# Kernel tuning notes

Hardware: AMD Instinct MI355X
Metric: run time of the kernel (lower is better)

The kernel has to match this reference:

```python
import jax, jax.numpy as jnp
import numpy as np

B, S, HID = 2, 2048, 1024
H, HKV, D = 16, 8, 128
G = H // HKV
EPS = 1e-6
ROPE_BASE = 1e6


def _rms_norm(x, w):
    # per-last-dim RMSNorm in fp32, matching QwenRMSNorm
    x32 = x.astype(jnp.float32)
    var = jnp.mean(x32 * x32, axis=-1, keepdims=True)
    return w * (x32 * jax.lax.rsqrt(var + EPS)).astype(x.dtype)


def _rotate_half(x):
    half = x.shape[-1] // 2
    return jnp.concatenate([-x[..., half:], x[..., :half]], axis=-1)


def setup_inputs() -> dict:
    key = jax.random.key(0)
    ks = jax.random.split(key, 6)
    return {
        "hidden_states": jax.random.normal(ks[0], (B, S, HID), dtype=jnp.float32),
        "position_ids": jnp.arange(S, dtype=jnp.int32),
        "Wq": jax.random.normal(ks[1], (HID, H * D), dtype=jnp.float32) * 0.02,
        "Wk": jax.random.normal(ks[2], (HID, HKV * D), dtype=jnp.float32) * 0.02,
        "Wv": jax.random.normal(ks[3], (HID, HKV * D), dtype=jnp.float32) * 0.02,
        "Wo": jax.random.normal(ks[4], (H * D, HID), dtype=jnp.float32) * 0.02,
        "q_norm_w": jnp.ones((D,), dtype=jnp.float32),
        "k_norm_w": jnp.ones((D,), dtype=jnp.float32),
    }


def reference(hidden_states, position_ids, Wq, Wk, Wv, Wo, q_norm_w, k_norm_w):
    b, s, _ = hidden_states.shape
    # projections
    q = (hidden_states @ Wq).reshape(b, s, H, D)
    k = (hidden_states @ Wk).reshape(b, s, HKV, D)
    v = (hidden_states @ Wv).reshape(b, s, HKV, D)
    # QK RMSNorm (per head_dim), then [B, heads, S, D]
    q = _rms_norm(q, q_norm_w).transpose(0, 2, 1, 3)
    k = _rms_norm(k, k_norm_w).transpose(0, 2, 1, 3)
    v = v.transpose(0, 2, 1, 3)
    # RoPE
    inv_freq = 1.0 / (ROPE_BASE ** (jnp.arange(0, D, 2, dtype=jnp.float32) / D))
    freqs = position_ids.astype(jnp.float32)[:, None] * inv_freq[None, :]  # [S, D/2]
    emb = jnp.concatenate([freqs, freqs], axis=-1)  # [S, D]
    cos = jnp.cos(emb)[None, None, :, :].astype(q.dtype)
    sin = jnp.sin(emb)[None, None, :, :].astype(q.dtype)
    q = q * cos + _rotate_half(q) * sin
    k = k * cos + _rotate_half(k) * sin
    # GQA attention without materializing repeated K/V:
    # q heads h = kh*G + g  <->  repeat_interleave(G, dim=1) of kv heads
    qg = q.reshape(b, HKV, G, s, D)
    scale = 1.0 / jnp.sqrt(jnp.asarray(D, dtype=q.dtype))
    scores = jnp.einsum('bhgqd,bhkd->bhgqk', qg, k) * scale  # [B,HKV,G,S,S]
    causal = jnp.tril(jnp.ones((s, s), dtype=bool))
    scores = jnp.where(causal[None, None, None, :, :], scores, jnp.finfo(scores.dtype).min)
    probs = jax.nn.softmax(scores, axis=-1)
    attn = jnp.einsum('bhgqk,bhkd->bhgqd', probs, v)  # [B,HKV,G,S,D]
    attn = attn.reshape(b, H, s, D).transpose(0, 2, 1, 3).reshape(b, s, H * D)
    out = attn @ Wo
    return out, k, v
```

## Files before the change

### kernel.cpp

```cpp
#include <hip/hip_runtime.h>

#define B_ 2
#define S_ 2048
#define HID_ 1024
#define H_ 16
#define HKV_ 8
#define D_ 128

typedef unsigned short u16;
typedef __attribute__((ext_vector_type(8))) short short8;
typedef __attribute__((ext_vector_type(4))) float f32x4;
typedef __attribute__((ext_vector_type(16))) float f32x16;
typedef __attribute__((ext_vector_type(2))) unsigned short u16x2;
typedef __attribute__((ext_vector_type(4))) unsigned short u16x4;
typedef const __attribute__((address_space(1))) void gvoid;
typedef __attribute__((address_space(3))) void svoid;

__device__ __forceinline__ u16 f2b(float f) {
  union { float f; unsigned u; } v; v.f = f;
  unsigned r = v.u + 0x7FFFu + ((v.u >> 16) & 1u);
  return (u16)(r >> 16);
}
__device__ __forceinline__ float b2f(u16 x) {
  union { unsigned u; float f; } v; v.u = ((unsigned)x) << 16; return v.f;
}

__device__ __forceinline__ float exp2_fast(float x) {
  float r; asm("v_exp_f32 %0, %1" : "=v"(r) : "v"(x)); return r;
}
__device__ __forceinline__ unsigned cvtpk_bf16(float lo, float hi) {
  unsigned r; asm("v_cvt_pk_bf16_f32 %0, %1, %2" : "=v"(r) : "v"(lo), "v"(hi)); return r;
}
__device__ __forceinline__ void vm_drain() {
  asm volatile("s_waitcnt vmcnt(0)" ::: "memory");
  __builtin_amdgcn_sched_barrier(0);
}

__global__ __launch_bounds__(256) void conv_bf16_kernel(const float* __restrict__ X,
                                                        u16* __restrict__ Y, int n4) {
  int i = blockIdx.x * 256 + threadIdx.x;
  if (i < n4) {
    const float4 v = ((const float4*)X)[i];
    u16x4 o = { f2b(v.x), f2b(v.y), f2b(v.z), f2b(v.w) };
    ((u16x4*)Y)[i] = o;
  }
}

template <bool PERM>
__global__ __launch_bounds__(256) void transpose_bf16_kernel(const float* __restrict__ W,
                                                             u16* __restrict__ Wt,
                                                             int K, int N) {
  __shared__ float t[32][33];
  const int nb = N >> 5;
  const int bx = blockIdx.x % nb;
  const int by = blockIdx.x / nb;
  const int tx = threadIdx.x & 31, ty = threadIdx.x >> 5;
#pragma unroll
  for (int i = 0; i < 32; i += 8)
    t[ty + i][tx] = W[(size_t)(by * 32 + ty + i) * N + bx * 32 + tx];
  __syncthreads();
#pragma unroll
  for (int i = 0; i < 32; i += 8) {
    int n = bx * 32 + ty + i;
    int nn;
    if (PERM) {
      int head = n >> 7, d = n & 127;
      int p = (d & 15) | (((d >> 6) & 1) << 4) | (((d >> 4) & 1) << 5) | (((d >> 5) & 1) << 6);
      nn = head * 128 + p;
    } else {
      nn = n;
    }
    Wt[(size_t)nn * K + by * 32 + tx] = f2b(t[tx][ty + i]);
  }
}

__global__ __launch_bounds__(256) void rope_table_kernel(const int* __restrict__ pid,
                                                         float* __restrict__ ct,
                                                         float* __restrict__ st) {
  int i = blockIdx.x * 256 + threadIdx.x;
  if (i >= 64 * S_) return;
  int f = i >> 11, s = i & 2047;
  double inv = exp2(-(double)f * (19.931568569324174 / 64.0));
  double ang = (double)pid[s] * inv;
  ct[i] = (float)cos(ang);
  st[i] = (float)sin(ang);
}

template <int M, int N, int K, int BM>
__global__ __launch_bounds__(256) void gemm_bt(const u16* __restrict__ A,
                                               const u16* __restrict__ Bt,
                                               float* __restrict__ C) {
  __shared__ u16 As[BM * 32];
  __shared__ u16 Bs[128 * 32];
  const int tid = threadIdx.x;
  const int w = tid >> 6;
  const int l = tid & 63;
  const int l15 = l & 15, lg = l >> 4;
  const int nbx = N / 128;
  const int bx = blockIdx.x % nbx, by = blockIdx.x / nbx;
  const int row0 = by * BM, col0 = bx * 128;
  const int wr = w >> 1, wc = w & 1;
  constexpr int MR = BM / 32;

  f32x4 acc[MR][4];
#pragma unroll
  for (int m = 0; m < MR; ++m)
#pragma unroll
    for (int n = 0; n < 4; ++n) acc[m][n] = (f32x4){0.f, 0.f, 0.f, 0.f};

  for (int k0 = 0; k0 < K; k0 += 32) {
    __syncthreads();
#pragma unroll
    for (int i = 0; i < BM / 64; ++i) {
      int c = i * 256 + tid;
      int r = c >> 2, cc = c & 3;
      const u16* sa = A + (size_t)(row0 + r) * K + k0 + cc * 8;
      __builtin_amdgcn_global_load_lds((gvoid*)sa, (svoid*)(As + (i * 256 + w * 64) * 8), 16, 0, 0);
    }
#pragma unroll
    for (int i = 0; i < 2; ++i) {
      int c = i * 256 + tid;
      int r = c >> 2, cc = c & 3;
      const u16* sb = Bt + (size_t)(col0 + r) * K + k0 + cc * 8;
      __builtin_amdgcn_global_load_lds((gvoid*)sb, (svoid*)(Bs + (i * 256 + w * 64) * 8), 16, 0, 0);
    }
    vm_drain();
    __syncthreads();
    short8 af[MR], bf[4];
#pragma unroll
    for (int m = 0; m < MR; ++m)
      af[m] = *(const short8*)(As + (wr * (BM / 2) + m * 16 + l15) * 32 + lg * 8);
#pragma unroll
    for (int n = 0; n < 4; ++n)
      bf[n] = *(const short8*)(Bs + (wc * 64 + n * 16 + l15) * 32 + lg * 8);
#pragma unroll
    for (int m = 0; m < MR; ++m)
#pragma unroll
      for (int n = 0; n < 4; ++n)
        acc[m][n] = __builtin_amdgcn_mfma_f32_16x16x32_bf16(af[m], bf[n], acc[m][n], 0, 0, 0);
  }
#pragma unroll
  for (int m = 0; m < MR; ++m)
#pragma unroll
    for (int n = 0; n < 4; ++n) {
      float* cp = C + (size_t)(row0 + wr * (BM / 2) + m * 16 + lg * 4) * N + col0 + wc * 64 + n * 16 + l15;
#pragma unroll
      for (int r = 0; r < 4; ++r) cp[(size_t)r * N] = acc[m][n][r];
    }
}

__global__ __launch_bounds__(256) void gemm_qkv_fused(const u16* __restrict__ A,
                                                      const u16* __restrict__ Bt,
                                                      const float* __restrict__ qnw,
                                                      const float* __restrict__ knw,
                                                      const float* __restrict__ ct_t,
                                                      const float* __restrict__ st_t,
                                                      u16* __restrict__ Qbb,
                                                      u16* __restrict__ Kbb,
                                                      float* __restrict__ kout,
                                                      float* __restrict__ vout) {
  constexpr int K = 1024;
  __shared__ u16 As[64 * 32];
  __shared__ u16 Bs[128 * 32];
  __shared__ float red[64][2];
  const int tid = threadIdx.x;
  const int w = tid >> 6;
  const int l = tid & 63;
  const int l15 = l & 15, lg = l >> 4;
  const int bx = blockIdx.x & 31, by = blockIdx.x >> 5;
  const int row0 = by * 64, col0 = bx * 128;
  const int wr = w >> 1, wc = w & 1;

  f32x4 acc[2][4];
#pragma unroll
  for (int m = 0; m < 2; ++m)
#pragma unroll
    for (int n = 0; n < 4; ++n) acc[m][n] = (f32x4){0.f, 0.f, 0.f, 0.f};

  for (int k0 = 0; k0 < K; k0 += 32) {
    __syncthreads();
    {
      int c = tid;
      int r = c >> 2, cc = c & 3;
      const u16* sa = A + (size_t)(row0 + r) * K + k0 + cc * 8;
      __builtin_amdgcn_global_load_lds((gvoid*)sa, (svoid*)(As + (w * 64) * 8), 16, 0, 0);
    }
#pragma unroll
    for (int i = 0; i < 2; ++i) {
      int c = i * 256 + tid;
      int r = c >> 2, cc = c & 3;
      const u16* sb = Bt + (size_t)(col0 + r) * K + k0 + cc * 8;
      __builtin_amdgcn_global_load_lds((gvoid*)sb, (svoid*)(Bs + (i * 256 + w * 64) * 8), 16, 0, 0);
    }
    vm_drain();
    __syncthreads();
    short8 af[2], bf[4];
#pragma unroll
    for (int m = 0; m < 2; ++m)
      af[m] = *(const short8*)(As + (wr * 32 + m * 16 + l15) * 32 + lg * 8);
#pragma unroll
    for (int n = 0; n < 4; ++n)
      bf[n] = *(const short8*)(Bs + (wc * 64 + n * 16 + l15) * 32 + lg * 8);
#pragma unroll
    for (int m = 0; m < 2; ++m)
#pragma unroll
      for (int n = 0; n < 4; ++n)
        acc[m][n] = __builtin_amdgcn_mfma_f32_16x16x32_bf16(af[m], bf[n], acc[m][n], 0, 0, 0);
  }

  const int b_ = row0 >> 11;
  const int s0 = row0 & 2047;
  if (bx < 24) {
    float part[2][4];
#pragma unroll
    for (int m = 0; m < 2; ++m)
#pragma unroll
      for (int r = 0; r < 4; ++r) {
        float p = 0.f;
#pragma unroll
        for (int n = 0; n < 4; ++n) p += acc[m][n][r] * acc[m][n][r];
        part[m][r] = p;
      }
#pragma unroll
    for (int i = 1; i < 16; i <<= 1)
#pragma unroll
      for (int m = 0; m < 2; ++m)
#pragma unroll
        for (int r = 0; r < 4; ++r) part[m][r] += __shfl_xor(part[m][r], i, 64);
    if (l15 == 0) {
#pragma unroll
      for (int m = 0; m < 2; ++m)
#pragma unroll
        for (int r = 0; r < 4; ++r) red[wr * 32 + m * 16 + lg * 4 + r][wc] = part[m][r];
    }
    __syncthreads();

    const bool isQ = bx < 16;
    const int h = isQ ? bx : bx - 16;
    const float* nw = isQ ? qnw : knw;
    u16* outb = isQ ? Qbb : Kbb;
    const int NH = isQ ? 16 : 8;
#pragma unroll
    for (int np = 0; np < 2; ++np) {
      const int d_lo = l15 + 32 * wc + 16 * np;
      const float w_lo = nw[d_lo], w_hi = nw[d_lo + 64];
#pragma unroll
      for (int m = 0; m < 2; ++m) {
        const int sb = s0 + wr * 32 + m * 16 + lg * 4;
        const float4 cv = *(const float4*)(ct_t + d_lo * 2048 + sb);
        const float4 sv = *(const float4*)(st_t + d_lo * 2048 + sb);
#pragma unroll
        for (int r = 0; r < 4; ++r) {
          const int ro = wr * 32 + m * 16 + lg * 4 + r;
          const float tot = red[ro][0] + red[ro][1];
          const float rms = rsqrtf(tot * (1.0f / 128.0f) + 1e-6f);
          const float xl = acc[m][2 * np][r] * rms * w_lo;
          const float xh = acc[m][2 * np + 1][r] * rms * w_hi;
          const float cc = ((const float*)&cv)[r], ss = ((const float*)&sv)[r];
          const float ol = xl * cc - xh * ss;
          const float oh = xh * cc + xl * ss;
          const size_t base = ((size_t)(b_ * NH + h) * 2048 + sb + r) * 128;
          outb[base + d_lo] = f2b(ol);
          outb[base + d_lo + 64] = f2b(oh);
          if (!isQ) {
            kout[base + d_lo] = ol;
            kout[base + d_lo + 64] = oh;
          }
        }
      }
    }
  } else {
    const int h = bx - 24;
#pragma unroll
    for (int n = 0; n < 4; ++n) {
      const int d = wc * 64 + n * 16 + l15;
#pragma unroll
      for (int m = 0; m < 2; ++m) {
        const int sb = s0 + wr * 32 + m * 16 + lg * 4;
#pragma unroll
        for (int r = 0; r < 4; ++r)
          vout[((size_t)(b_ * 8 + h) * 2048 + sb + r) * 128 + d] = acc[m][n][r];
      }
    }
  }
}

__global__ __launch_bounds__(256) void vtrans2_kernel(const float* __restrict__ vout,
                                                      u16* __restrict__ VTb) {
  __shared__ float t[32][33];
  const int bid = blockIdx.x;
  const int stile = bid & 63;
  const int dt = (bid >> 6) & 3;
  const int bh = bid >> 8;
  const int tx = threadIdx.x & 31, ty = threadIdx.x >> 5;
#pragma unroll
  for (int j = 0; j < 4; ++j) {
    int s = stile * 32 + ty + 8 * j;
    t[ty + 8 * j][tx] = vout[((size_t)bh * 2048 + s) * 128 + dt * 32 + tx];
  }
  __syncthreads();
#pragma unroll
  for (int j = 0; j < 4; ++j) {
    int d = dt * 32 + ty + 8 * j;
    VTb[((size_t)bh * 128 + d) * 2048 + stile * 32 + tx] = f2b(t[tx][ty + 8 * j]);
  }
}

__global__ __launch_bounds__(256, 2) void attn_kernel(const u16* __restrict__ Qb,
                                                      const u16* __restrict__ Kb,
                                                      const u16* __restrict__ VTb,
                                                      u16* __restrict__ Ab,
                                                      u16* __restrict__ Op,
                                                      float* __restrict__ Ml) {
  __shared__ u16 lds[2][16384];
  const int tid = threadIdx.x;
  const int w = tid >> 6, l = tid & 63;
  const int l31 = l & 31, hi = l >> 5;
  const int bid = blockIdx.x;
  const int half = bid & 1;
  const int pid = bid >> 1;
  const int b = pid >> 7;
  const int hh = (pid >> 3) & 15;
  const int p8 = pid & 7;
  const int hkv = hh >> 1;

  const u16* Kh = Kb + (size_t)(b * HKV_ + hkv) * S_ * 128;
  const u16* VTh = VTb + (size_t)(b * HKV_ + hkv) * 128 * S_;
  const float KSC = 0.12751740027f;
  int cur = 0;

  auto stage = [&](int kt, int buf) {
    const u16* Kp = Kh + (size_t)kt * 64 * 128;
    const u16* Vp = VTh + kt * 64;
    u16* Kd = &lds[buf][0];
    u16* Vd = &lds[buf][8192];
#pragma unroll
    for (int i = 0; i < 4; ++i) {
      int c = i * 256 + tid;
      int kr = c >> 4, kc = c & 15;
      int kcs = kc ^ ((kr ^ (kr >> 3)) & 15);
      __builtin_amdgcn_global_load_lds((gvoid*)(Kp + kr * 128 + kcs * 8),
                                       (svoid*)(Kd + (i * 256 + w * 64) * 8), 16, 0, 0);
      int vd = c >> 3, vc = c & 7;
      int vcs = vc ^ ((vd ^ (vd >> 3)) & 7);
      __builtin_amdgcn_global_load_lds((gvoid*)(Vp + (size_t)vd * S_ + vcs * 8),
                                       (svoid*)(Vd + (i * 256 + w * 64) * 8), 16, 0, 0);
    }
  };

  auto run_seg = [&](int pp, int kt0, int kt1, int mode) {
    const int q0 = pp * 128;
    const int ntp = 2 * (pp + 1);
    const int qrow = q0 + w * 32 + l31;

    short8 qf[8];
    {
      const u16* qp = Qb + ((size_t)(b * H_ + hh) * S_ + qrow) * 128 + hi * 8;
#pragma unroll
      for (int c = 0; c < 8; ++c) qf[c] = *(const short8*)(qp + c * 16);
    }

    float m_run = -1e30f, l_run = 0.f;
    f32x16 oacc[4];
#pragma unroll
    for (int n = 0; n < 4; ++n)
#pragma unroll
      for (int r = 0; r < 16; ++r) oacc[n][r] = 0.f;

    stage(kt0, cur);
    vm_drain();
    __syncthreads();
    for (int kt = kt0; kt < kt1; ++kt) {
      if (kt + 1 < kt1) stage(kt + 1, cur ^ 1);
      const u16* Kl = &lds[cur][0];
      const u16* Vl = &lds[cur][8192];
      const bool domask = (kt >= ntp - 2);

#pragma unroll
      for (int ts = 0; ts < 2; ++ts) {
        f32x16 stv;
#pragma unroll
        for (int r = 0; r < 16; ++r) stv[r] = 0.f;
        {
          const int row = ts * 32 + l31;
          const int rb = row * 256, sw = ((row ^ (row >> 3)) & 15) << 4;
#pragma unroll
          for (int c = 0; c < 8; ++c) {
            short8 kf = *(const short8*)((const char*)Kl + rb + ((c * 32 + hi * 16) ^ sw));
            stv = __builtin_amdgcn_mfma_f32_32x32x16_bf16(kf, qf[c], stv, 0, 0, 0);
          }
        }

        float pvv[16];
        float mx = -1e30f;
#pragma unroll
        for (int r = 0; r < 16; ++r) {
          float x = stv[r] * KSC;
          if (domask) {
            int kv = kt * 64 + ts * 32 + (r & 3) + 8 * (r >> 2) + 4 * hi;
            if (kv > qrow) x = -1e30f;
          }
          pvv[r] = x;
          mx = fmaxf(mx, x);
        }
        mx = fmaxf(mx, __shfl_xor(mx, 32, 64));

        if (__any(mx > m_run + 8.0f)) {
          float mnew = fmaxf(m_run, mx);
          float corr = exp2_fast(m_run - mnew);
          l_run *= corr;
          m_run = mnew;
#pragma unroll
          for (int r = 0; r < 16; ++r) {
            float cr = __shfl(corr, (r & 3) + 8 * (r >> 2) + 4 * hi, 64);
#pragma unroll
            for (int n = 0; n < 4; ++n) oacc[n][r] *= cr;
          }
        }

        float ls = 0.f;
#pragma unroll
        for (int r = 0; r < 16; ++r) {
          float p = exp2_fast(pvv[r] - m_run);
          pvv[r] = p;
          ls += p;
        }
        l_run += ls + __shfl_xor(ls, 32, 64);

        unsigned W[4][2], Wx[4][2];
#pragma unroll
        for (int g = 0; g < 4; ++g)
#pragma unroll
          for (int i = 0; i < 2; ++i) {
            W[g][i] = cvtpk_bf16(pvv[4 * g + 2 * i], pvv[4 * g + 2 * i + 1]);
            Wx[g][i] = __shfl_xor(W[g][i], 32, 64);
          }

#pragma unroll
        for (int cc = 0; cc < 2; ++cc) {
          short8 paf;
          ((unsigned*)&paf)[0] = hi ? Wx[2 * cc + 1][0] : W[2 * cc][0];
          ((unsigned*)&paf)[1] = hi ? Wx[2 * cc + 1][1] : W[2 * cc][1];
          ((unsigned*)&paf)[2] = hi ? W[2 * cc + 1][0] : Wx[2 * cc][0];
          ((unsigned*)&paf)[3] = hi ? W[2 * cc + 1][1] : Wx[2 * cc][1];
          const int cp = ts * 2 + cc;
#pragma unroll
          for (int n = 0; n < 4; ++n) {
            const int d = n * 32 + l31;
            const int swv = ((d ^ (d >> 3)) & 7) << 4;
            short8 vf = *(const short8*)((const char*)Vl + d * 128 + ((cp * 32 + hi * 16) ^ swv));
            oacc[n] = __builtin_amdgcn_mfma_f32_32x32x16_bf16(paf, vf, oacc[n], 0, 0, 0);
          }
        }
      }
      vm_drain();
      __syncthreads();
      cur ^= 1;
    }

    if (mode == 0) {
#pragma unroll
      for (int r = 0; r < 16; ++r) {
        const int ql = (r & 3) + 8 * (r >> 2) + 4 * hi;
        float lb = __shfl(l_run, ql, 64);
        float inv = 1.0f / lb;
        const int q = q0 + w * 32 + ql;
        u16* op = Ab + ((size_t)(b * S_) + q) * 2048 + hh * 128 + l31;
#pragma unroll
        for (int n = 0; n < 4; ++n) op[n * 32] = f2b(oacc[n][r] * inv);
      }
    } else {
      const int part = mode - 1;
      u16* ob = Op + ((size_t)(part * 256 + pid)) * 128 * 128;
#pragma unroll
      for (int r = 0; r < 16; ++r) {
        const int ql = (r & 3) + 8 * (r >> 2) + 4 * hi;
        const int qq = w * 32 + ql;
#pragma unroll
        for (int n = 0; n < 4; ++n) ob[qq * 128 + n * 32 + l31] = f2b(oacc[n][r]);
      }
      if (hi == 0) {
        float* mlb = Ml + ((size_t)(part * 256 + pid)) * 256;
        mlb[w * 32 + l31] = m_run;
        mlb[128 + w * 32 + l31] = l_run;
      }
    }
  };

  if (half == 0) {
    run_seg(p8, 0, 2 * p8 + 2, 0);
    run_seg(15 - p8, 0, 15 - 2 * p8, 1);
  } else {
    run_seg(15 - p8, 15 - 2 * p8, 32 - 2 * p8, 2);
  }
}

__global__ __launch_bounds__(256) void attn_combine_kernel(const u16* __restrict__ Op,
                                                           const float* __restrict__ Ml,
                                                           u16* __restrict__ Ab) {
  const int pid = blockIdx.x;
  const int b = pid >> 7, hh = (pid >> 3) & 15, p8 = pid & 7;
  const int pp = 15 - p8;
  const int q = threadIdx.x >> 1;
  const int d0 = (threadIdx.x & 1) * 64;
  const float* ml0 = Ml + (size_t)pid * 256;
  const float* ml1 = Ml + (size_t)(256 + pid) * 256;
  const float m0 = ml0[q], l0 = ml0[128 + q];
  const float m1 = ml1[q], l1 = ml1[128 + q];
  const float m = fmaxf(m0, m1);
  const float w0 = exp2_fast(m0 - m), w1 = exp2_fast(m1 - m);
  const float linv = 1.0f / (w0 * l0 + w1 * l1);
  const u16* o0 = Op + ((size_t)pid * 128 + q) * 128 + d0;
  const u16* o1 = Op + ((size_t)(256 + pid) * 128 + q) * 128 + d0;
  u16* ab = Ab + ((size_t)(b * S_) + pp * 128 + q) * 2048 + hh * 128 + d0;
#pragma unroll
  for (int c = 0; c < 8; ++c) {
    short8 a = *(const short8*)(o0 + c * 8);
    short8 bb = *(const short8*)(o1 + c * 8);
    short8 o;
#pragma unroll
    for (int j = 0; j < 8; ++j)
      o[j] = (short)f2b((w0 * b2f((u16)a[j]) + w1 * b2f((u16)bb[j])) * linv);
    *(short8*)(ab + c * 8) = o;
  }
}

extern "C" void kernel_launch(void* const* d_in, const int* in_sizes, int n_in,
                              void* d_out, int out_size, void* d_ws, size_t ws_size,
                              hipStream_t stream) {
  const float* hs  = (const float*)d_in[0];
  const int*   pid = (const int*)d_in[1];
  const float* Wq  = (const float*)d_in[2];
  const float* Wk  = (const float*)d_in[3];
  const float* Wv  = (const float*)d_in[4];
  const float* Wo  = (const float*)d_in[5];
  const float* qnw = (const float*)d_in[6];
  const float* knw = (const float*)d_in[7];

  float* out0 = (float*)d_out;
  float* kout = out0 + (size_t)B_ * HKV_ * S_ * D_;
  float* vout = kout + (size_t)B_ * HKV_ * S_ * D_;

  char* ws = (char*)d_ws;
  size_t off = 0;
  auto alloc = [&](size_t bytes) {
    void* p = ws + off;
    off += (bytes + 255) & ~(size_t)255;
    return p;
  };
  u16*   Xb    = (u16*)alloc((size_t)4096 * 1024 * 2);
  u16*   Wqkvt = (u16*)alloc((size_t)4096 * 1024 * 2);
  u16*   Wot   = (u16*)alloc((size_t)1024 * 2048 * 2);
  float* ct_t  = (float*)alloc((size_t)64 * 2048 * 4);
  float* st_t  = (float*)alloc((size_t)64 * 2048 * 4);
  u16*   Qbb   = (u16*)alloc((size_t)B_ * H_ * S_ * D_ * 2);
  u16*   Kbb   = (u16*)alloc((size_t)B_ * HKV_ * S_ * D_ * 2);
  u16*   VTb   = (u16*)alloc((size_t)B_ * HKV_ * D_ * S_ * 2);
  u16*   Ab    = (u16*)alloc((size_t)B_ * S_ * H_ * D_ * 2);
  u16*   Op    = (u16*)alloc((size_t)2 * 256 * 128 * 128 * 2);
  float* Ml    = (float*)alloc((size_t)2 * 256 * 256 * 4);

  conv_bf16_kernel<<<4096, 256, 0, stream>>>(hs, Xb, 4096 * 1024 / 4);
  transpose_bf16_kernel<true><<<(2048 / 32) * (1024 / 32), 256, 0, stream>>>(Wq, Wqkvt, 1024, 2048);
  transpose_bf16_kernel<true><<<(1024 / 32) * (1024 / 32), 256, 0, stream>>>(Wk, Wqkvt + (size_t)2048 * 1024, 1024, 1024);
  transpose_bf16_kernel<false><<<(1024 / 32) * (1024 / 32), 256, 0, stream>>>(Wv, Wqkvt + (size_t)3072 * 1024, 1024, 1024);
  transpose_bf16_kernel<false><<<(1024 / 32) * (2048 / 32), 256, 0, stream>>>(Wo, Wot, 2048, 1024);
  rope_table_kernel<<<512, 256, 0, stream>>>(pid, ct_t, st_t);

  gemm_qkv_fused<<<2048, 256, 0, stream>>>(Xb, Wqkvt, qnw, knw, ct_t, st_t,
                                           Qbb, Kbb, kout, vout);
  vtrans2_kernel<<<4096, 256, 0, stream>>>(vout, VTb);

  attn_kernel<<<512, 256, 0, stream>>>(Qbb, Kbb, VTb, Ab, Op, Ml);
  attn_combine_kernel<<<256, 256, 0, stream>>>(Op, Ml, Ab);

  gemm_bt<4096, 1024, 2048, 64><<<8 * 64, 256, 0, stream>>>(Ab, Wot, out0);
}
```

Before: 189.4 us.

## Fuse V transpose into QKV GEMM, double its K-tile with swizzled LDS, prioritize attention MFMA

The V-transpose kernel is removed; the QKV GEMM epilogue now writes bf16 V transposed directly as packed 4-element stores, which saves a launch and a full reread of the fp32 V buffer. The QKV GEMM's K-step grows from 32 to 64 with an XOR-swizzled LDS layout, halving the number of barrier and drain iterations and avoiding bank conflicts. The attention kernel wraps its MFMA sections in s_setprio to favour matrix issue across waves. The transposed V stores are only 8-byte strided writes, so they may coalesce poorly.

Result: faster. 173.6 us (-8.4%).

```diff
diff --git a/kernel.cpp b/kernel.cpp
--- a/kernel.cpp
+++ b/kernel.cpp
@@ -158,10 +158,11 @@
                                                       u16* __restrict__ Qbb,
                                                       u16* __restrict__ Kbb,
                                                       float* __restrict__ kout,
-                                                      float* __restrict__ vout) {
+                                                      float* __restrict__ vout,
+                                                      u16* __restrict__ VTb) {
   constexpr int K = 1024;
-  __shared__ u16 As[64 * 32];
-  __shared__ u16 Bs[128 * 32];
+  __shared__ u16 As[64 * 64];
+  __shared__ u16 Bs[128 * 64];
   __shared__ float red[64][2];
   const int tid = threadIdx.x;
   const int w = tid >> 6;
@@ -177,35 +178,47 @@
 #pragma unroll
     for (int n = 0; n < 4; ++n) acc[m][n] = (f32x4){0.f, 0.f, 0.f, 0.f};
 
-  for (int k0 = 0; k0 < K; k0 += 32) {
+  for (int k0 = 0; k0 < K; k0 += 64) {
     __syncthreads();
-    {
-      int c = tid;
-      int r = c >> 2, cc = c & 3;
-      const u16* sa = A + (size_t)(row0 + r) * K + k0 + cc * 8;
-      __builtin_amdgcn_global_load_lds((gvoid*)sa, (svoid*)(As + (w * 64) * 8), 16, 0, 0);
-    }
 #pragma unroll
     for (int i = 0; i < 2; ++i) {
       int c = i * 256 + tid;
-      int r = c >> 2, cc = c & 3;
-      const u16* sb = Bt + (size_t)(col0 + r) * K + k0 + cc * 8;
+      int r = c >> 3, cc = c & 7;
+      int cs = cc ^ ((r ^ (r >> 3)) & 7);
+      const u16* sa = A + (size_t)(row0 + r) * K + k0 + cs * 8;
+      __builtin_amdgcn_global_load_lds((gvoid*)sa, (svoid*)(As + (i * 256 + w * 64) * 8), 16, 0, 0);
+    }
+#pragma unroll
+    for (int i = 0; i < 4; ++i) {
+      int c = i * 256 + tid;
+      int r = c >> 3, cc = c & 7;
+      int cs = cc ^ ((r ^ (r >> 3)) & 7);
+      const u16* sb = Bt + (size_t)(col0 + r) * K + k0 + cs * 8;
       __builtin_amdgcn_global_load_lds((gvoid*)sb, (svoid*)(Bs + (i * 256 + w * 64) * 8), 16, 0, 0);
     }
     vm_drain();
     __syncthreads();
-    short8 af[2], bf[4];
-#pragma unroll
-    for (int m = 0; m < 2; ++m)
-      af[m] = *(const short8*)(As + (wr * 32 + m * 16 + l15) * 32 + lg * 8);
-#pragma unroll
-    for (int n = 0; n < 4; ++n)
-      bf[n] = *(const short8*)(Bs + (wc * 64 + n * 16 + l15) * 32 + lg * 8);
-#pragma unroll
-    for (int m = 0; m < 2; ++m)
-#pragma unroll
-      for (int n = 0; n < 4; ++n)
-        acc[m][n] = __builtin_amdgcn_mfma_f32_16x16x32_bf16(af[m], bf[n], acc[m][n], 0, 0, 0);
+#pragma unroll
+    for (int kk = 0; kk < 2; ++kk) {
+      short8 af[2], bf[4];
+#pragma unroll
+      for (int m = 0; m < 2; ++m) {
+        const int row = wr * 32 + m * 16 + l15;
+        af[m] = *(const short8*)((const char*)As + row * 128 +
+                                 (((kk * 4 + lg) ^ ((row ^ (row >> 3)) & 7)) << 4));
+      }
+#pragma unroll
+      for (int n = 0; n < 4; ++n) {
+        const int row = wc * 64 + n * 16 + l15;
+        bf[n] = *(const short8*)((const char*)Bs + row * 128 +
+                                 (((kk * 4 + lg) ^ ((row ^ (row >> 3)) & 7)) << 4));
+      }
+#pragma unroll
+      for (int m = 0; m < 2; ++m)
+#pragma unroll
+        for (int n = 0; n < 4; ++n)
+          acc[m][n] = __builtin_amdgcn_mfma_f32_16x16x32_bf16(af[m], bf[n], acc[m][n], 0, 0, 0);
+    }
   }
 
   const int b_ = row0 >> 11;
@@ -277,32 +290,16 @@
 #pragma unroll
       for (int m = 0; m < 2; ++m) {
         const int sb = s0 + wr * 32 + m * 16 + lg * 4;
-#pragma unroll
-        for (int r = 0; r < 4; ++r)
-          vout[((size_t)(b_ * 8 + h) * 2048 + sb + r) * 128 + d] = acc[m][n][r];
-      }
-    }
-  }
-}
-
-__global__ __launch_bounds__(256) void vtrans2_kernel(const float* __restrict__ vout,
-                                                      u16* __restrict__ VTb) {
-  __shared__ float t[32][33];
-  const int bid = blockIdx.x;
-  const int stile = bid & 63;
-  const int dt = (bid >> 6) & 3;
-  const int bh = bid >> 8;
-  const int tx = threadIdx.x & 31, ty = threadIdx.x >> 5;
-#pragma unroll
-  for (int j = 0; j < 4; ++j) {
-    int s = stile * 32 + ty + 8 * j;
-    t[ty + 8 * j][tx] = vout[((size_t)bh * 2048 + s) * 128 + dt * 32 + tx];
-  }
-  __syncthreads();
-#pragma unroll
-  for (int j = 0; j < 4; ++j) {
-    int d = dt * 32 + ty + 8 * j;
-    VTb[((size_t)bh * 128 + d) * 2048 + stile * 32 + tx] = f2b(t[tx][ty + 8 * j]);
+        u16x4 pk;
+#pragma unroll
+        for (int r = 0; r < 4; ++r) {
+          const float x = acc[m][n][r];
+          vout[((size_t)(b_ * 8 + h) * 2048 + sb + r) * 128 + d] = x;
+          pk[r] = f2b(x);
+        }
+        *(u16x4*)(VTb + ((size_t)(b_ * 8 + h) * 128 + d) * 2048 + sb) = pk;
+      }
+    }
   }
 }
 
@@ -384,11 +381,13 @@
         {
           const int row = ts * 32 + l31;
           const int rb = row * 256, sw = ((row ^ (row >> 3)) & 15) << 4;
+          __builtin_amdgcn_s_setprio(1);
 #pragma unroll
           for (int c = 0; c < 8; ++c) {
             short8 kf = *(const short8*)((const char*)Kl + rb + ((c * 32 + hi * 16) ^ sw));
             stv = __builtin_amdgcn_mfma_f32_32x32x16_bf16(kf, qf[c], stv, 0, 0, 0);
           }
+          __builtin_amdgcn_s_setprio(0);
         }
 
         float pvv[16];
@@ -436,6 +435,7 @@
             Wx[g][i] = __shfl_xor(W[g][i], 32, 64);
           }
 
+        __builtin_amdgcn_s_setprio(1);
 #pragma unroll
         for (int cc = 0; cc < 2; ++cc) {
           short8 paf;
@@ -452,6 +452,7 @@
             oacc[n] = __builtin_amdgcn_mfma_f32_32x32x16_bf16(paf, vf, oacc[n], 0, 0, 0);
           }
         }
+        __builtin_amdgcn_s_setprio(0);
       }
       vm_drain();
       __syncthreads();
@@ -568,8 +569,7 @@
   rope_table_kernel<<<512, 256, 0, stream>>>(pid, ct_t, st_t);
 
   gemm_qkv_fused<<<2048, 256, 0, stream>>>(Xb, Wqkvt, qnw, knw, ct_t, st_t,
-                                           Qbb, Kbb, kout, vout);
-  vtrans2_kernel<<<4096, 256, 0, stream>>>(vout, VTb);
+                                           Qbb, Kbb, kout, vout, VTb);
 
   attn_kernel<<<512, 256, 0, stream>>>(Qbb, Kbb, VTb, Ab, Op, Ml);
   attn_combine_kernel<<<256, 256, 0, stream>>>(Op, Ml, Ab);
```
